# Performance work log

Hardware: AMD Instinct MI355X
Metric: run time of the kernel (lower is better)

The kernel has to match this reference:

```python
import jax, jax.numpy as jnp
import numpy as np

B, L, D, F, E, K = 2, 2048, 1024, 4096, 8, 2


def setup_inputs() -> dict:
    key = jax.random.key(0)
    ks = jax.random.split(key, 8)
    s = 0.02
    return {
        "x": jax.random.normal(ks[0], (B, L, D), dtype=jnp.float32),
        "Wg": jax.random.normal(ks[1], (D, E), dtype=jnp.float32) * s,
        "bg": jnp.zeros((E,), dtype=jnp.float32),
        "W1": jax.random.normal(ks[2], (E, D, F), dtype=jnp.float32) * s,
        "b1": jnp.zeros((E, F), dtype=jnp.float32),
        "W2": jax.random.normal(ks[3], (E, F, D), dtype=jnp.float32) * s,
        "b2": jnp.zeros((E, D), dtype=jnp.float32),
    }


def reference(x, Wg, bg, W1, b1, W2, b2):
    num_experts = Wg.shape[1]
    gate_scores = x @ Wg + bg                                # [B,L,E]
    topk_scores, topk_ids = jax.lax.top_k(gate_scores, K)    # [B,L,K]
    topk_weights = jax.nn.softmax(topk_scores, axis=-1)      # [B,L,K]
    gate_probs = jax.nn.softmax(gate_scores, axis=-1)        # [B,L,E]

    onehot = jax.nn.one_hot(topk_ids, num_experts, dtype=x.dtype)  # [B,L,K,E]
    expert_mask = onehot.sum(axis=2)                         # [B,L,E]
    freq = expert_mask.mean(axis=(0, 1))                     # [E]
    prob_mean = gate_probs.mean(axis=(0, 1))                 # [E]
    load_balance_loss = num_experts * jnp.sum(freq * prob_mean)

    # combine weight per token per expert (0 if expert not selected)
    combine = jnp.sum(onehot * topk_weights[..., None], axis=2)    # [B,L,E]

    # dense dispatch: run every expert FFN on all tokens, weight & combine
    h = jnp.einsum('bld,edf->belf', x, W1) + b1[None, :, None, :]  # [B,E,L,F]
    h = jax.nn.gelu(h, approximate=False)                          # exact GELU (torch default)
    y = jnp.einsum('belf,efd->beld', h, W2) + b2[None, :, None, :] # [B,E,L,D]
    out = jnp.einsum('ble,beld->bld', combine, y)                  # [B,L,D]
    return out, load_balance_loss
```

## Files before the change

kernel.cpp:

```cpp
#include <hip/hip_runtime.h>
#include <hip/hip_bf16.h>
#include <cstdint>
#include <cstddef>

#define B_ 2
#define L_ 2048
#define D_ 1024
#define F_ 4096
#define E_ 8
#define NTOK 4096
#define MAXROWS 9216

typedef __hip_bfloat16 bf16;
typedef __attribute__((ext_vector_type(8))) short short8;
typedef __attribute__((ext_vector_type(4))) float floatx4;

typedef const __attribute__((address_space(1))) uint32_t* gptr_t;
typedef __attribute__((address_space(3))) uint32_t* lptr_t;

__device__ __forceinline__ void async_load16(const bf16* gp, bf16* lp) {
    __builtin_amdgcn_global_load_lds((gptr_t)(const void*)gp, (lptr_t)(void*)lp, 16, 0, 0);
}

__device__ __forceinline__ uint16_t bfbits(bf16 h) {
    union { bf16 b; uint16_t u; } v; v.b = h; return v.u;
}
__device__ __forceinline__ uint32_t pack2(float a, float b) {
    return (uint32_t)bfbits(__float2bfloat16(a)) | ((uint32_t)bfbits(__float2bfloat16(b)) << 16);
}

__global__ __launch_bounds__(256) void gate_kernel(
    const float* __restrict__ x, const float* __restrict__ Wg,
    const float* __restrict__ bg, float* __restrict__ psum_pad,
    uint32_t* __restrict__ top_ids, float* __restrict__ top_w)
{
    __shared__ float psum_l[E_];
    int t = threadIdx.x;
    if (t < E_) psum_l[t] = 0.f;
    __syncthreads();

    int wave = t >> 6, lane = t & 63;
    for (int j = 0; j < 4; ++j) {
        int token = blockIdx.x * 16 + wave * 4 + j;
        const float* xr = x + (size_t)token * D_;

        float acc[E_];
#pragma unroll
        for (int e = 0; e < E_; ++e) acc[e] = 0.f;
        for (int i = 0; i < D_/64; ++i) {
            int d = lane + 64*i;
            float xv = xr[d];
            const float4* wr4 = (const float4*)(Wg + (size_t)d * E_);
            float4 wa = wr4[0], wb = wr4[1];
            acc[0] += xv * wa.x;  acc[1] += xv * wa.y;
            acc[2] += xv * wa.z;  acc[3] += xv * wa.w;
            acc[4] += xv * wb.x;  acc[5] += xv * wb.y;
            acc[6] += xv * wb.z;  acc[7] += xv * wb.w;
        }
#pragma unroll
        for (int off = 32; off >= 1; off >>= 1) {
#pragma unroll
            for (int e = 0; e < E_; ++e) acc[e] += __shfl_xor(acc[e], off, 64);
        }
        if (lane == 0) {
            float s[E_];
#pragma unroll
            for (int e = 0; e < E_; ++e) s[e] = acc[e] + bg[e];
            int i0 = 0;
#pragma unroll
            for (int e = 1; e < E_; ++e) if (s[e] > s[i0]) i0 = e;
            int i1 = -1;
#pragma unroll
            for (int e = 0; e < E_; ++e) {
                if (e == i0) continue;
                if (i1 < 0 || s[e] > s[i1]) i1 = e;
            }
            float e1 = expf(s[i1] - s[i0]);
            float w0 = 1.f / (1.f + e1);
            float w1 = e1 * w0;
            top_ids[token] = (uint32_t)i0 | ((uint32_t)i1 << 8);
            top_w[token]        = w0;
            top_w[NTOK + token] = w1;

            float mx = s[i0], p[E_], sum = 0.f;
#pragma unroll
            for (int e = 0; e < E_; ++e) { p[e] = expf(s[e] - mx); sum += p[e]; }
            float inv = 1.f / sum;
#pragma unroll
            for (int e = 0; e < E_; ++e) atomicAdd(&psum_l[e], p[e] * inv);
        }
    }
    __syncthreads();
    if (t < E_) atomicAdd(&psum_pad[t * 32], psum_l[t]);
}

__global__ __launch_bounds__(256) void compact_kernel(
    const uint32_t* __restrict__ top_ids, const float* __restrict__ top_w,
    int* __restrict__ cnt, int* __restrict__ tok_list, float* __restrict__ w_list)
{
    int e = blockIdx.x;
    int t = threadIdx.x, wave = t >> 6, lane = t & 63;
    __shared__ int wcnt[4];
    int base = 0;
    for (int r0 = 0; r0 < NTOK; r0 += 256) {
        int token = r0 + t;
        uint32_t ids = top_ids[token];
        int slot = -1;
        if ((int)(ids & 255u) == e) slot = 0;
        else if ((int)((ids >> 8) & 255u) == e) slot = 1;
        unsigned long long mask = __ballot(slot >= 0);
        int lpos = __popcll(mask & ((1ull << lane) - 1ull));
        if (lane == 0) wcnt[wave] = (int)__popcll(mask);
        __syncthreads();
        int woff = 0, tot = 0;
#pragma unroll
        for (int w2 = 0; w2 < 4; ++w2) { if (w2 < wave) woff += wcnt[w2]; tot += wcnt[w2]; }
        if (slot >= 0) {
            int pos = base + woff + lpos;
            tok_list[e*NTOK + pos] = token;
            w_list[e*NTOK + pos]   = top_w[slot*NTOK + token];
        }
        base += tot;
        __syncthreads();
    }
    if (t == 0) cnt[e] = base;
}

__global__ void finalize_gate_kernel(const int* __restrict__ cnt, const float* __restrict__ psum_pad,
                                     int* __restrict__ off, float* __restrict__ loss_out)
{
    int o = 0; float Ls = 0.f;
    for (int e = 0; e < E_; ++e) {
        off[e] = o;
        o += (cnt[e] + 127) & ~127;
        Ls += (float)cnt[e] * psum_pad[e * 32];
    }
    loss_out[0] = (float)E_ * Ls / ((float)NTOK * (float)NTOK);
}

__global__ __launch_bounds__(256) void transpose_bf16_kernel(
    const float* __restrict__ in, bf16* __restrict__ outp, int R, int C)
{
    int tilesR = R >> 6, tilesC = C >> 6;
    int per = tilesR * tilesC;
    int bx = blockIdx.x;
    int e  = bx / per; int r2 = bx % per;
    int tr = r2 / tilesC, tc = r2 % tilesC;
    int r0 = tr << 6, c0 = tc << 6;
    const float* ip = in  + (size_t)e * R * C;
    bf16*       op = outp + (size_t)e * R * C;

    __shared__ bf16 tile[64][65];
    int t = threadIdx.x;
    int tx = t & 15, ty = t >> 4;
#pragma unroll
    for (int i = 0; i < 4; ++i) {
        int r = ty + (i << 4);
        float4 v = *(const float4*)(ip + (size_t)(r0 + r) * C + c0 + tx*4);
        tile[r][tx*4+0] = __float2bfloat16(v.x);
        tile[r][tx*4+1] = __float2bfloat16(v.y);
        tile[r][tx*4+2] = __float2bfloat16(v.z);
        tile[r][tx*4+3] = __float2bfloat16(v.w);
    }
    __syncthreads();
#pragma unroll
    for (int i = 0; i < 4; ++i) {
        int c = ty + (i << 4);
        uint2 uu;
        uu.x = (uint32_t)bfbits(tile[tx*4+0][c]) | ((uint32_t)bfbits(tile[tx*4+1][c]) << 16);
        uu.y = (uint32_t)bfbits(tile[tx*4+2][c]) | ((uint32_t)bfbits(tile[tx*4+3][c]) << 16);
        *(uint2*)(op + (size_t)(c0 + c) * R + r0 + tx*4) = uu;
    }
}

__global__ __launch_bounds__(256) void gather_kernel(
    const float* __restrict__ x, const int* __restrict__ cnt, const int* __restrict__ off,
    const int* __restrict__ tok_list, bf16* __restrict__ Xg)
{
    int bx = blockIdx.x;
    int e  = bx >> 12;
    int i  = bx & 4095;
    if (i >= cnt[e]) return;
    int tok = tok_list[e*NTOK + i];
    size_t row = (size_t)(off[e] + i);
    int t = threadIdx.x;
    float4 v = *(const float4*)(x + (size_t)tok * D_ + t*4);
    uint2 uu;
    uu.x = pack2(v.x, v.y);
    uu.y = pack2(v.z, v.w);
    *(uint2*)(Xg + row * D_ + t*4) = uu;
}

__global__ __launch_bounds__(256) void gemm1_kernel(
    const bf16* __restrict__ Xg, const bf16* __restrict__ W1t,
    const float* __restrict__ b1, const int* __restrict__ cnt,
    const int* __restrict__ off, bf16* __restrict__ H)
{
    int bx = blockIdx.x;
    int e  = bx >> 10;
    int r2 = bx & 1023;
    int mtile = r2 >> 5, ntile = r2 & 31;
    int n = cnt[e];
    if (mtile * 128 >= n) return;
    int row0 = off[e] + mtile * 128;
    int f0 = ntile * 128;

    __shared__ bf16 As[128*64];
    __shared__ bf16 Bs[128*64];

    int t = threadIdx.x;
    int wave = t >> 6, lane = t & 63;
    int wm = wave & 1, wn = wave >> 1;
    int q = lane >> 4, ln = lane & 15;
    int sm = lane >> 3, sc = lane & 7;

    const bf16* Abase = Xg  + (size_t)row0 * D_;
    const bf16* Bbase = W1t + ((size_t)e * F_ + f0) * D_;

    floatx4 acc[4][4];
#pragma unroll
    for (int mt = 0; mt < 4; ++mt)
#pragma unroll
        for (int nt = 0; nt < 4; ++nt) acc[mt][nt] = {0.f, 0.f, 0.f, 0.f};

    for (int kt = 0; kt < D_; kt += 64) {
        __syncthreads();
#pragma unroll
        for (int i = 0; i < 4; ++i) {
            int g = wave*4 + i;
            int m = g*8 + sm;
            int ca = sc ^ (m & 7);
            async_load16(Abase + (size_t)m * D_ + kt + ca*8, &As[g*512]);
            async_load16(Bbase + (size_t)m * D_ + kt + ca*8, &Bs[g*512]);
        }
        __syncthreads();
#pragma unroll
        for (int kk = 0; kk < 2; ++kk) {
            short8 av[4], bv[4];
#pragma unroll
            for (int mt = 0; mt < 4; ++mt) {
                int r = wm*64 + mt*16 + ln;
                int cs = (kk*4 + q) ^ (r & 7);
                av[mt] = *(const short8*)&As[r*64 + cs*8];
            }
#pragma unroll
            for (int nt = 0; nt < 4; ++nt) {
                int r = wn*64 + nt*16 + ln;
                int cs = (kk*4 + q) ^ (r & 7);
                bv[nt] = *(const short8*)&Bs[r*64 + cs*8];
            }
#pragma unroll
            for (int mt = 0; mt < 4; ++mt)
#pragma unroll
                for (int nt = 0; nt < 4; ++nt)
                    acc[mt][nt] = __builtin_amdgcn_mfma_f32_16x16x32_bf16(av[mt], bv[nt], acc[mt][nt], 0, 0, 0);
        }
    }

    const float is2 = 0.70710678118654752f;
#pragma unroll
    for (int nt = 0; nt < 4; ++nt) {
        int f = f0 + wn*64 + nt*16 + ln;
        float b1v = b1[(size_t)e * F_ + f];
#pragma unroll
        for (int mt = 0; mt < 4; ++mt) {
            int rl = wm*64 + mt*16 + q*4;
#pragma unroll
            for (int r = 0; r < 4; ++r) {
                float v = acc[mt][nt][r] + b1v;
                v = 0.5f * v * (1.f + erff(v * is2));
                H[(size_t)(row0 + rl + r) * F_ + f] = __float2bfloat16(v);
            }
        }
    }
}

__global__ __launch_bounds__(256) void gemm2_kernel(
    const bf16* __restrict__ H, const bf16* __restrict__ W2t,
    const float* __restrict__ b2, const int* __restrict__ cnt, const int* __restrict__ off,
    const int* __restrict__ tok_list, const float* __restrict__ w_list,
    float* __restrict__ out)
{
    int bx = blockIdx.x;
    int e  = bx >> 8;
    int r2 = bx & 255;
    int mtile = r2 >> 3, ntile = r2 & 7;
    int n = cnt[e];
    if (mtile * 128 >= n) return;
    int row0 = off[e] + mtile * 128;
    int d0 = ntile * 128;

    __shared__ bf16 As[128*64];
    __shared__ bf16 Bs[128*64];

    int t = threadIdx.x;
    int wave = t >> 6, lane = t & 63;
    int wm = wave & 1, wn = wave >> 1;
    int q = lane >> 4, ln = lane & 15;
    int sm = lane >> 3, sc = lane & 7;

    const bf16* Abase = H   + (size_t)row0 * F_;
    const bf16* Bbase = W2t + ((size_t)e * D_ + d0) * F_;

    floatx4 acc[4][4];
#pragma unroll
    for (int mt = 0; mt < 4; ++mt)
#pragma unroll
        for (int nt = 0; nt < 4; ++nt) acc[mt][nt] = {0.f, 0.f, 0.f, 0.f};

    for (int kt = 0; kt < F_; kt += 64) {
        __syncthreads();
#pragma unroll
        for (int i = 0; i < 4; ++i) {
            int g = wave*4 + i;
            int m = g*8 + sm;
            int ca = sc ^ (m & 7);
            async_load16(Abase + (size_t)m * F_ + kt + ca*8, &As[g*512]);
            async_load16(Bbase + (size_t)m * F_ + kt + ca*8, &Bs[g*512]);
        }
        __syncthreads();
#pragma unroll
        for (int kk = 0; kk < 2; ++kk) {
            short8 av[4], bv[4];
#pragma unroll
            for (int mt = 0; mt < 4; ++mt) {
                int r = wm*64 + mt*16 + ln;
                int cs = (kk*4 + q) ^ (r & 7);
                av[mt] = *(const short8*)&As[r*64 + cs*8];
            }
#pragma unroll
            for (int nt = 0; nt < 4; ++nt) {
                int r = wn*64 + nt*16 + ln;
                int cs = (kk*4 + q) ^ (r & 7);
                bv[nt] = *(const short8*)&Bs[r*64 + cs*8];
            }
#pragma unroll
            for (int mt = 0; mt < 4; ++mt)
#pragma unroll
                for (int nt = 0; nt < 4; ++nt)
                    acc[mt][nt] = __builtin_amdgcn_mfma_f32_16x16x32_bf16(av[mt], bv[nt], acc[mt][nt], 0, 0, 0);
        }
    }

    float b2v[4];
#pragma unroll
    for (int nt = 0; nt < 4; ++nt) b2v[nt] = b2[(size_t)e * D_ + d0 + wn*64 + nt*16 + ln];

#pragma unroll
    for (int mt = 0; mt < 4; ++mt) {
#pragma unroll
        for (int r = 0; r < 4; ++r) {
            int i = mtile*128 + wm*64 + mt*16 + q*4 + r;
            if (i < n) {
                int tok = tok_list[e*NTOK + i];
                float w = w_list[e*NTOK + i];
                float* op = out + (size_t)tok * D_;
#pragma unroll
                for (int nt = 0; nt < 4; ++nt) {
                    int d = d0 + wn*64 + nt*16 + ln;
                    atomicAdd(op + d, w * (acc[mt][nt][r] + b2v[nt]));
                }
            }
        }
    }
}

extern "C" void kernel_launch(void* const* d_in, const int* in_sizes, int n_in,
                              void* d_out, int out_size, void* d_ws, size_t ws_size,
                              hipStream_t stream)
{
    const float* x  = (const float*)d_in[0];
    const float* Wg = (const float*)d_in[1];
    const float* bg = (const float*)d_in[2];
    const float* W1 = (const float*)d_in[3];
    const float* b1 = (const float*)d_in[4];
    const float* W2 = (const float*)d_in[5];
    const float* b2 = (const float*)d_in[6];
    float* out = (float*)d_out;

    char* ws = (char*)d_ws;
    int*      cnt      = (int*)(ws + 0);
    int*      off      = (int*)(ws + 128);
    float*    psum_pad = (float*)(ws + 1024);
    uint32_t* top_ids  = (uint32_t*)(ws + 8192);
    float*    top_w    = (float*)(ws + 8192 + 16384);
    int*      tok_list = (int*)(ws + 65536);
    float*    w_list   = (float*)(ws + 65536 + 131072);
    size_t o = 1u << 20;
    bf16*  W1t = (bf16*)(ws + o);  o += (size_t)E_ * D_ * F_ * 2;
    bf16*  W2t = (bf16*)(ws + o);  o += (size_t)E_ * F_ * D_ * 2;
    bf16*  Xg  = (bf16*)(ws + o);  o += (size_t)MAXROWS * D_ * 2;
    bf16*  H   = (bf16*)(ws + o);

    hipMemsetAsync(d_out, 0, (size_t)out_size * sizeof(float), stream);
    hipMemsetAsync(ws + 1024, 0, 1024, stream);

    transpose_bf16_kernel<<<E_ * 16 * 64, 256, 0, stream>>>(W1, W1t, D_, F_);
    transpose_bf16_kernel<<<E_ * 64 * 16, 256, 0, stream>>>(W2, W2t, F_, D_);

    gate_kernel<<<256, 256, 0, stream>>>(x, Wg, bg, psum_pad, top_ids, top_w);
    compact_kernel<<<E_, 256, 0, stream>>>(top_ids, top_w, cnt, tok_list, w_list);
    finalize_gate_kernel<<<1, 1, 0, stream>>>(cnt, psum_pad, off, out + (size_t)NTOK * D_);
    gather_kernel<<<E_ * 4096, 256, 0, stream>>>(x, cnt, off, tok_list, Xg);

    gemm1_kernel<<<E_ * 32 * 32, 256, 0, stream>>>(Xg, W1t, b1, cnt, off, H);
    gemm2_kernel<<<E_ * 32 * 8, 256, 0, stream>>>(H, W2t, b2, cnt, off, tok_list, w_list, out);
}
```

Baseline: 699.7 us.

## Split-K gemm2 across two blocks and drop LDS from weight transpose

The second expert GEMM is split along the F reduction dimension into two halves, each run by its own block. Both halves add their partial sums into the output atomically, and only the first half adds the bias. This doubles the number of blocks to improve occupancy across CUs, at the cost of twice as many atomic adds. Separately, the weight transpose/convert kernel now transposes a 4x4 register tile per thread instead of going through shared memory with a sync. Its global writes become smaller, more strided stores.

```diff
diff --git a/kernel.cpp b/kernel.cpp
--- a/kernel.cpp
+++ b/kernel.cpp
@@ -148,29 +148,29 @@
     int tr = r2 / tilesC, tc = r2 % tilesC;
     int r0 = tr << 6, c0 = tc << 6;
     const float* ip = in  + (size_t)e * R * C;
-    bf16*       op = outp + (size_t)e * R * C;
-
-    __shared__ bf16 tile[64][65];
+    bf16*        op = outp + (size_t)e * R * C;
+
     int t = threadIdx.x;
-    int tx = t & 15, ty = t >> 4;
-#pragma unroll
-    for (int i = 0; i < 4; ++i) {
-        int r = ty + (i << 4);
-        float4 v = *(const float4*)(ip + (size_t)(r0 + r) * C + c0 + tx*4);
-        tile[r][tx*4+0] = __float2bfloat16(v.x);
-        tile[r][tx*4+1] = __float2bfloat16(v.y);
-        tile[r][tx*4+2] = __float2bfloat16(v.z);
-        tile[r][tx*4+3] = __float2bfloat16(v.w);
-    }
-    __syncthreads();
-#pragma unroll
-    for (int i = 0; i < 4; ++i) {
-        int c = ty + (i << 4);
-        uint2 uu;
-        uu.x = (uint32_t)bfbits(tile[tx*4+0][c]) | ((uint32_t)bfbits(tile[tx*4+1][c]) << 16);
-        uu.y = (uint32_t)bfbits(tile[tx*4+2][c]) | ((uint32_t)bfbits(tile[tx*4+3][c]) << 16);
-        *(uint2*)(op + (size_t)(c0 + c) * R + r0 + tx*4) = uu;
-    }
+    int c = (t & 15) * 4;
+    int r = (t >> 4) * 4;
+
+    const float* p0 = ip + (size_t)(r0 + r) * C + c0 + c;
+    float4 v0 = *(const float4*)(p0);
+    float4 v1 = *(const float4*)(p0 + C);
+    float4 v2 = *(const float4*)(p0 + 2*C);
+    float4 v3 = *(const float4*)(p0 + 3*C);
+
+    uint2 o0, o1, o2, o3;
+    o0.x = pack2(v0.x, v1.x);  o0.y = pack2(v2.x, v3.x);
+    o1.x = pack2(v0.y, v1.y);  o1.y = pack2(v2.y, v3.y);
+    o2.x = pack2(v0.z, v1.z);  o2.y = pack2(v2.z, v3.z);
+    o3.x = pack2(v0.w, v1.w);  o3.y = pack2(v2.w, v3.w);
+
+    bf16* q = op + (size_t)(c0 + c) * R + r0 + r;
+    *(uint2*)(q)       = o0;
+    *(uint2*)(q + R)   = o1;
+    *(uint2*)(q + 2*R) = o2;
+    *(uint2*)(q + 3*R) = o3;
 }
 
 __global__ __launch_bounds__(256) void gather_kernel(
@@ -282,13 +282,16 @@
     float* __restrict__ out)
 {
     int bx = blockIdx.x;
-    int e  = bx >> 8;
-    int r2 = bx & 255;
-    int mtile = r2 >> 3, ntile = r2 & 7;
+    int e   = bx >> 9;
+    int rem = bx & 511;
+    int mtile = rem >> 4;
+    int ntile = (rem >> 1) & 7;
+    int ks    = rem & 1;
     int n = cnt[e];
     if (mtile * 128 >= n) return;
     int row0 = off[e] + mtile * 128;
     int d0 = ntile * 128;
+    int kt0 = ks * (F_/2);
 
     __shared__ bf16 As[128*64];
     __shared__ bf16 Bs[128*64];
@@ -308,7 +311,7 @@
 #pragma unroll
         for (int nt = 0; nt < 4; ++nt) acc[mt][nt] = {0.f, 0.f, 0.f, 0.f};
 
-    for (int kt = 0; kt < F_; kt += 64) {
+    for (int kt = kt0; kt < kt0 + F_/2; kt += 64) {
         __syncthreads();
 #pragma unroll
         for (int i = 0; i < 4; ++i) {
@@ -344,7 +347,8 @@
 
     float b2v[4];
 #pragma unroll
-    for (int nt = 0; nt < 4; ++nt) b2v[nt] = b2[(size_t)e * D_ + d0 + wn*64 + nt*16 + ln];
+    for (int nt = 0; nt < 4; ++nt)
+        b2v[nt] = (ks == 0) ? b2[(size_t)e * D_ + d0 + wn*64 + nt*16 + ln] : 0.f;
 
 #pragma unroll
     for (int mt = 0; mt < 4; ++mt) {
@@ -404,5 +408,5 @@
     gather_kernel<<<E_ * 4096, 256, 0, stream>>>(x, cnt, off, tok_list, Xg);
 
     gemm1_kernel<<<E_ * 32 * 32, 256, 0, stream>>>(Xg, W1t, b1, cnt, off, H);
-    gemm2_kernel<<<E_ * 32 * 8, 256, 0, stream>>>(H, W2t, b2, cnt, off, tok_list, w_list, out);
-}
+    gemm2_kernel<<<E_ * 32 * 8 * 2, 256, 0, stream>>>(H, W2t, b2, cnt, off, tok_list, w_list, out);
+}
```

New measurement: 699.7 us. Within noise of the previous version (+0.0%).

## Replace gemm2 atomic scatter with bf16 Y buffer and per-token combine kernel

Applied to the files above, without the earlier changes.

gemm2 now writes per-expert outputs (with bias) as bf16 rows into a Y buffer that reuses the Xg workspace, instead of doing weighted atomicAdds into the output. A new combine kernel reads each token's two expert rows through a rowid map built in compact_kernel and writes the weighted sum directly, which also removes the output memset. The weight transpose kernel is rewritten to convert and transpose in registers, with each thread handling 8 rows, instead of going through shared memory. Rounding Y to bf16 adds a small precision loss, and the extra pass costs a Y write and read.

```diff
diff --git a/kernel.cpp b/kernel.cpp
--- a/kernel.cpp
+++ b/kernel.cpp
@@ -28,6 +28,8 @@
 __device__ __forceinline__ uint32_t pack2(float a, float b) {
     return (uint32_t)bfbits(__float2bfloat16(a)) | ((uint32_t)bfbits(__float2bfloat16(b)) << 16);
 }
+__device__ __forceinline__ float ublo(uint32_t u){ return __uint_as_float(u << 16); }
+__device__ __forceinline__ float ubhi(uint32_t u){ return __uint_as_float(u & 0xffff0000u); }
 
 __global__ __launch_bounds__(256) void gate_kernel(
     const float* __restrict__ x, const float* __restrict__ Wg,
@@ -96,7 +98,8 @@
 
 __global__ __launch_bounds__(256) void compact_kernel(
     const uint32_t* __restrict__ top_ids, const float* __restrict__ top_w,
-    int* __restrict__ cnt, int* __restrict__ tok_list, float* __restrict__ w_list)
+    int* __restrict__ cnt, int* __restrict__ tok_list, float* __restrict__ w_list,
+    int* __restrict__ rowid)
 {
     int e = blockIdx.x;
     int t = threadIdx.x, wave = t >> 6, lane = t & 63;
@@ -119,6 +122,7 @@
             int pos = base + woff + lpos;
             tok_list[e*NTOK + pos] = token;
             w_list[e*NTOK + pos]   = top_w[slot*NTOK + token];
+            rowid[slot*NTOK + token] = (e << 13) | pos;
         }
         base += tot;
         __syncthreads();
@@ -141,35 +145,33 @@
 __global__ __launch_bounds__(256) void transpose_bf16_kernel(
     const float* __restrict__ in, bf16* __restrict__ outp, int R, int C)
 {
-    int tilesR = R >> 6, tilesC = C >> 6;
+    int tilesR = R >> 7, tilesC = C >> 6;
     int per = tilesR * tilesC;
     int bx = blockIdx.x;
     int e  = bx / per; int r2 = bx % per;
     int tr = r2 / tilesC, tc = r2 % tilesC;
-    int r0 = tr << 6, c0 = tc << 6;
+    int r0 = tr << 7, c0 = tc << 6;
     const float* ip = in  + (size_t)e * R * C;
-    bf16*       op = outp + (size_t)e * R * C;
-
-    __shared__ bf16 tile[64][65];
-    int t = threadIdx.x;
-    int tx = t & 15, ty = t >> 4;
+    bf16*        op = outp + (size_t)e * R * C;
+
+    int t = threadIdx.x;
+    int c = (t & 15) * 4;
+    int r = (t >> 4) * 8;
+
+    const float* p = ip + (size_t)(r0 + r) * C + c0 + c;
+    float4 v[8];
+#pragma unroll
+    for (int j = 0; j < 8; ++j) v[j] = *(const float4*)(p + (size_t)j * C);
+    const float* vf = (const float*)v;
+
 #pragma unroll
     for (int i = 0; i < 4; ++i) {
-        int r = ty + (i << 4);
-        float4 v = *(const float4*)(ip + (size_t)(r0 + r) * C + c0 + tx*4);
-        tile[r][tx*4+0] = __float2bfloat16(v.x);
-        tile[r][tx*4+1] = __float2bfloat16(v.y);
-        tile[r][tx*4+2] = __float2bfloat16(v.z);
-        tile[r][tx*4+3] = __float2bfloat16(v.w);
-    }
-    __syncthreads();
-#pragma unroll
-    for (int i = 0; i < 4; ++i) {
-        int c = ty + (i << 4);
-        uint2 uu;
-        uu.x = (uint32_t)bfbits(tile[tx*4+0][c]) | ((uint32_t)bfbits(tile[tx*4+1][c]) << 16);
-        uu.y = (uint32_t)bfbits(tile[tx*4+2][c]) | ((uint32_t)bfbits(tile[tx*4+3][c]) << 16);
-        *(uint2*)(op + (size_t)(c0 + c) * R + r0 + tx*4) = uu;
+        uint4 o;
+        o.x = pack2(vf[0*4+i], vf[1*4+i]);
+        o.y = pack2(vf[2*4+i], vf[3*4+i]);
+        o.z = pack2(vf[4*4+i], vf[5*4+i]);
+        o.w = pack2(vf[6*4+i], vf[7*4+i]);
+        *(uint4*)(op + (size_t)(c0 + c + i) * R + r0 + r) = o;
     }
 }
 
@@ -278,13 +280,13 @@
 __global__ __launch_bounds__(256) void gemm2_kernel(
     const bf16* __restrict__ H, const bf16* __restrict__ W2t,
     const float* __restrict__ b2, const int* __restrict__ cnt, const int* __restrict__ off,
-    const int* __restrict__ tok_list, const float* __restrict__ w_list,
-    float* __restrict__ out)
+    bf16* __restrict__ Y)
 {
     int bx = blockIdx.x;
-    int e  = bx >> 8;
-    int r2 = bx & 255;
-    int mtile = r2 >> 3, ntile = r2 & 7;
+    int e   = bx >> 8;
+    int rem = bx & 255;
+    int mtile = rem >> 3;
+    int ntile = rem & 7;
     int n = cnt[e];
     if (mtile * 128 >= n) return;
     int row0 = off[e] + mtile * 128;
@@ -344,25 +346,44 @@
 
     float b2v[4];
 #pragma unroll
-    for (int nt = 0; nt < 4; ++nt) b2v[nt] = b2[(size_t)e * D_ + d0 + wn*64 + nt*16 + ln];
+    for (int nt = 0; nt < 4; ++nt)
+        b2v[nt] = b2[(size_t)e * D_ + d0 + wn*64 + nt*16 + ln];
 
 #pragma unroll
     for (int mt = 0; mt < 4; ++mt) {
 #pragma unroll
         for (int r = 0; r < 4; ++r) {
-            int i = mtile*128 + wm*64 + mt*16 + q*4 + r;
+            int loc = wm*64 + mt*16 + q*4 + r;
+            int i = mtile*128 + loc;
             if (i < n) {
-                int tok = tok_list[e*NTOK + i];
-                float w = w_list[e*NTOK + i];
-                float* op = out + (size_t)tok * D_;
-#pragma unroll
-                for (int nt = 0; nt < 4; ++nt) {
-                    int d = d0 + wn*64 + nt*16 + ln;
-                    atomicAdd(op + d, w * (acc[mt][nt][r] + b2v[nt]));
-                }
-            }
-        }
-    }
+                bf16* yp = Y + (size_t)(row0 + loc) * D_ + d0;
+#pragma unroll
+                for (int nt = 0; nt < 4; ++nt)
+                    yp[wn*64 + nt*16 + ln] = __float2bfloat16(acc[mt][nt][r] + b2v[nt]);
+            }
+        }
+    }
+}
+
+__global__ __launch_bounds__(256) void combine_kernel(
+    const bf16* __restrict__ Y, const int* __restrict__ rowid,
+    const float* __restrict__ top_w, const int* __restrict__ off,
+    float* __restrict__ out)
+{
+    int tok = blockIdx.x;
+    int t = threadIdx.x;
+    int v0 = rowid[tok], v1 = rowid[NTOK + tok];
+    float w0 = top_w[tok], w1 = top_w[NTOK + tok];
+    size_t r0 = (size_t)(off[v0 >> 13] + (v0 & 8191));
+    size_t r1 = (size_t)(off[v1 >> 13] + (v1 & 8191));
+    uint2 a = *(const uint2*)(Y + r0 * D_ + t*4);
+    uint2 b = *(const uint2*)(Y + r1 * D_ + t*4);
+    float4 o;
+    o.x = w0 * ublo(a.x) + w1 * ublo(b.x);
+    o.y = w0 * ubhi(a.x) + w1 * ubhi(b.x);
+    o.z = w0 * ublo(a.y) + w1 * ublo(b.y);
+    o.w = w0 * ubhi(a.y) + w1 * ubhi(b.y);
+    *(float4*)(out + (size_t)tok * D_ + t*4) = o;
 }
 
 extern "C" void kernel_launch(void* const* d_in, const int* in_sizes, int n_in,
@@ -386,23 +407,25 @@
     float*    top_w    = (float*)(ws + 8192 + 16384);
     int*      tok_list = (int*)(ws + 65536);
     float*    w_list   = (float*)(ws + 65536 + 131072);
+    int*      rowid    = (int*)(ws + 327680);
     size_t o = 1u << 20;
     bf16*  W1t = (bf16*)(ws + o);  o += (size_t)E_ * D_ * F_ * 2;
     bf16*  W2t = (bf16*)(ws + o);  o += (size_t)E_ * F_ * D_ * 2;
     bf16*  Xg  = (bf16*)(ws + o);  o += (size_t)MAXROWS * D_ * 2;
     bf16*  H   = (bf16*)(ws + o);
-
-    hipMemsetAsync(d_out, 0, (size_t)out_size * sizeof(float), stream);
+    bf16*  Y   = Xg;
+
     hipMemsetAsync(ws + 1024, 0, 1024, stream);
 
-    transpose_bf16_kernel<<<E_ * 16 * 64, 256, 0, stream>>>(W1, W1t, D_, F_);
-    transpose_bf16_kernel<<<E_ * 64 * 16, 256, 0, stream>>>(W2, W2t, F_, D_);
+    transpose_bf16_kernel<<<E_ * 8 * 64, 256, 0, stream>>>(W1, W1t, D_, F_);
+    transpose_bf16_kernel<<<E_ * 32 * 16, 256, 0, stream>>>(W2, W2t, F_, D_);
 
     gate_kernel<<<256, 256, 0, stream>>>(x, Wg, bg, psum_pad, top_ids, top_w);
-    compact_kernel<<<E_, 256, 0, stream>>>(top_ids, top_w, cnt, tok_list, w_list);
+    compact_kernel<<<E_, 256, 0, stream>>>(top_ids, top_w, cnt, tok_list, w_list, rowid);
     finalize_gate_kernel<<<1, 1, 0, stream>>>(cnt, psum_pad, off, out + (size_t)NTOK * D_);
     gather_kernel<<<E_ * 4096, 256, 0, stream>>>(x, cnt, off, tok_list, Xg);
 
     gemm1_kernel<<<E_ * 32 * 32, 256, 0, stream>>>(Xg, W1t, b1, cnt, off, H);
-    gemm2_kernel<<<E_ * 32 * 8, 256, 0, stream>>>(H, W2t, b2, cnt, off, tok_list, w_list, out);
-}
+    gemm2_kernel<<<E_ * 32 * 8, 256, 0, stream>>>(H, W2t, b2, cnt, off, Y);
+    combine_kernel<<<NTOK, 256, 0, stream>>>(Y, rowid, top_w, off, out);
+}
```

After: 684.6 us. 1.02x faster.
